# Kernel tuning notes

Measured on AMD Instinct MI355X. Metric: run time of the kernel, lower is better.

Reference implementation:

```python
import jax, jax.numpy as jnp
import numpy as np

N = 100000
E = 1600000
IN_C = 256
HID = 128
OUT_C = 128
HEADS = 4
C_HEAD = HID // HEADS
BN_EPS = 1e-5
NEG_SLOPE = 0.2


def setup_inputs() -> dict:
    key = jax.random.key(0)
    ks = jax.random.split(key, 12)
    s = lambda fan: 1.0 / np.sqrt(fan)
    return {
        "x": jax.random.normal(ks[0], (N, IN_C), dtype=jnp.float32),
        "W_gat": jax.random.normal(ks[1], (IN_C, HID), dtype=jnp.float32) * s(IN_C),
        "att_src": jax.random.normal(ks[2], (HEADS, C_HEAD), dtype=jnp.float32) * s(C_HEAD),
        "att_dst": jax.random.normal(ks[3], (HEADS, C_HEAD), dtype=jnp.float32) * s(C_HEAD),
        "bias_gat": jnp.zeros((HID,), dtype=jnp.float32),
        "bn1_gamma": jnp.ones((HID,), dtype=jnp.float32),
        "bn1_beta": jnp.zeros((HID,), dtype=jnp.float32),
        "eps_gin": jnp.zeros((), dtype=jnp.float32),
        "lin_W": jax.random.normal(ks[4], (HID, OUT_C), dtype=jnp.float32) * s(HID),
        "lin_b": jnp.zeros((OUT_C,), dtype=jnp.float32),
        "bn2_gamma": jnp.ones((OUT_C,), dtype=jnp.float32),
        "bn2_beta": jnp.zeros((OUT_C,), dtype=jnp.float32),
        "edge_index": jax.random.randint(ks[5], (2, E), 0, N, dtype=jnp.int64),
    }


def batch_norm(h, gamma, beta):
    mu = jnp.mean(h, axis=0)
    var = jnp.var(h, axis=0)
    return (h - mu) * jax.lax.rsqrt(var + BN_EPS) * gamma + beta


def reference(x, W_gat, att_src, att_dst, bias_gat, bn1_gamma, bn1_beta,
              eps_gin, lin_W, lin_b, bn2_gamma, bn2_beta, edge_index):
    src, dst = edge_index[0], edge_index[1]
    # ---- GATConv ----
    h = (x @ W_gat).reshape(N, HEADS, C_HEAD)              # [N,H,C]
    a_src = jnp.einsum('nhc,hc->nh', h, att_src)            # [N,H]
    a_dst = jnp.einsum('nhc,hc->nh', h, att_dst)            # [N,H]
    e = jax.nn.leaky_relu(a_src[src] + a_dst[dst], NEG_SLOPE)  # [E,H]
    # segment softmax over incoming edges of each dst node
    m = jax.ops.segment_max(e, dst, num_segments=N)         # [N,H]
    num = jnp.exp(e - m[dst])                                # [E,H]
    den = jax.ops.segment_sum(num, dst, num_segments=N)      # [N,H]
    alpha = num / den[dst]                                   # [E,H]
    msg = alpha[:, :, None] * h[src]                         # [E,H,C]
    out1 = jax.ops.segment_sum(msg, dst, num_segments=N)     # [N,H,C]
    out1 = out1.reshape(N, HID) + bias_gat
    # BN + ELU (dropout = identity in eval)
    out1 = jax.nn.elu(batch_norm(out1, bn1_gamma, bn1_beta))
    # ---- GINConv: nn((1+eps)*x + sum_neighbors) ----
    agg = jax.ops.segment_sum(out1[src], dst, num_segments=N)
    z = (1.0 + eps_gin) * out1 + agg
    out2 = z @ lin_W + lin_b
    out2 = jax.nn.elu(batch_norm(out2, bn2_gamma, bn2_beta))
    return out2
```

## Files before the change

### kernel.cpp

```cpp
#include <hip/hip_runtime.h>

#define N_NODES 100000
#define N_EDGES 1600000
#define IN_C 256
#define HID 128
#define NEG_SLOPE 0.2f
#define BN_EPS 1e-5f
#define NBUCK 391
#define NPART 391
#define BPAD 5120
#define ELEM_BLOCKS 2048

typedef unsigned int uint32;
typedef __attribute__((ext_vector_type(8))) short bf16x8;
typedef __attribute__((ext_vector_type(4))) float f32x4;

__device__ __forceinline__ float lrelu(float x) { return x > 0.f ? x : NEG_SLOPE * x; }

__device__ __forceinline__ unsigned short f2bf(float f) {
    uint32 u = __float_as_uint(f);
    u += 0x7fffu + ((u >> 16) & 1u);
    return (unsigned short)(u >> 16);
}
__device__ __forceinline__ float bf2f(unsigned short h) {
    return __uint_as_float(((uint32)h) << 16);
}
__device__ __forceinline__ float bflo(uint32 v) { return __uint_as_float(v << 16); }
__device__ __forceinline__ float bfhi(uint32 v) { return __uint_as_float(v & 0xffff0000u); }
__device__ __forceinline__ uint32 packbf(float a, float b) {
    return (uint32)f2bf(a) | ((uint32)f2bf(b) << 16);
}

__global__ void k_transpose_all(const float* __restrict__ W1, const float* __restrict__ W2,
                                unsigned short* __restrict__ Wt1,
                                unsigned short* __restrict__ Wt2,
                                int* __restrict__ gcursor, float* __restrict__ bnacc) {
    int t = threadIdx.x;
    if (blockIdx.x == 0) {
        for (int i = t; i < NBUCK + 1; i += 256) gcursor[i] = 0;
        bnacc[t] = 0.f;
        bnacc[256 + t] = 0.f;
    }
    int idx = blockIdx.x * 256 + t;
    if (idx < IN_C * 128) {
        int k = idx >> 7, n = idx & 127;
        Wt1[n * IN_C + k] = f2bf(W1[idx]);
    } else {
        idx -= IN_C * 128;
        if (idx < HID * 128) {
            int k = idx >> 7, n = idx & 127;
            Wt2[n * HID + k] = f2bf(W2[idx]);
        }
    }
}

template <bool AF32, bool OUTF32, bool ATT, bool STATS>
__global__ __launch_bounds__(256) void k_gemm(const void* __restrict__ Av,
                                              const unsigned short* __restrict__ Wt,
                                              void* __restrict__ Out, int K,
                                              const float* __restrict__ att_s,
                                              const float* __restrict__ att_d,
                                              float* __restrict__ a_src,
                                              float* __restrict__ a_dst,
                                              float* __restrict__ bnst) {
    __shared__ unsigned short As[128 * 72];
    __shared__ unsigned short Bs[128 * 72];
    const int t = threadIdx.x;
    const int n0 = blockIdx.x * 128;
    const int wv = t >> 6, lane = t & 63;
    const int wy = wv >> 1, wx = wv & 1;
    const int lm = lane & 15, lg = lane >> 4;
    const float* Af = (const float*)Av;
    const unsigned short* Ah = (const unsigned short*)Av;

    f32x4 acc[4][4];
#pragma unroll
    for (int i = 0; i < 4; ++i)
#pragma unroll
        for (int j = 0; j < 4; ++j) acc[i][j] = (f32x4){0.f, 0.f, 0.f, 0.f};

    float4 afp[8];
    uint4 ahp[4];
    uint4 bvp[4];

    if (AF32) {
#pragma unroll
        for (int p = 0; p < 8; ++p) {
            int idx = p * 256 + t, row = idx >> 4, c4 = idx & 15, gn = n0 + row;
            afp[p] = (gn < N_NODES) ? *(const float4*)&Af[(size_t)gn * K + c4 * 4]
                                    : make_float4(0.f, 0.f, 0.f, 0.f);
        }
    } else {
#pragma unroll
        for (int p = 0; p < 4; ++p) {
            int idx = p * 256 + t, row = idx >> 3, c = idx & 7, gn = n0 + row;
            ahp[p] = (gn < N_NODES) ? *(const uint4*)&Ah[(size_t)gn * K + c * 8]
                                    : make_uint4(0, 0, 0, 0);
        }
    }
#pragma unroll
    for (int p = 0; p < 4; ++p) {
        int idx = p * 256 + t, n = idx >> 3, c = idx & 7;
        bvp[p] = *(const uint4*)&Wt[(size_t)n * K + c * 8];
    }

    for (int kc = 0; kc < K; kc += 64) {
        if (AF32) {
#pragma unroll
            for (int p = 0; p < 8; ++p) {
                int idx = p * 256 + t, row = idx >> 4, c4 = idx & 15;
                ushort4 b;
                b.x = f2bf(afp[p].x); b.y = f2bf(afp[p].y);
                b.z = f2bf(afp[p].z); b.w = f2bf(afp[p].w);
                *(ushort4*)&As[row * 72 + c4 * 4] = b;
            }
        } else {
#pragma unroll
            for (int p = 0; p < 4; ++p) {
                int idx = p * 256 + t, row = idx >> 3, c = idx & 7;
                *(uint4*)&As[row * 72 + c * 8] = ahp[p];
            }
        }
#pragma unroll
        for (int p = 0; p < 4; ++p) {
            int idx = p * 256 + t, n = idx >> 3, c = idx & 7;
            *(uint4*)&Bs[n * 72 + c * 8] = bvp[p];
        }
        __syncthreads();
        int kn = kc + 64;
        if (kn < K) {
            if (AF32) {
#pragma unroll
                for (int p = 0; p < 8; ++p) {
                    int idx = p * 256 + t, row = idx >> 4, c4 = idx & 15, gn = n0 + row;
                    afp[p] = (gn < N_NODES) ? *(const float4*)&Af[(size_t)gn * K + kn + c4 * 4]
                                            : make_float4(0.f, 0.f, 0.f, 0.f);
                }
            } else {
#pragma unroll
                for (int p = 0; p < 4; ++p) {
                    int idx = p * 256 + t, row = idx >> 3, c = idx & 7, gn = n0 + row;
                    ahp[p] = (gn < N_NODES) ? *(const uint4*)&Ah[(size_t)gn * K + kn + c * 8]
                                            : make_uint4(0, 0, 0, 0);
                }
            }
#pragma unroll
            for (int p = 0; p < 4; ++p) {
                int idx = p * 256 + t, n = idx >> 3, c = idx & 7;
                bvp[p] = *(const uint4*)&Wt[(size_t)n * K + kn + c * 8];
            }
        }
#pragma unroll
        for (int ks = 0; ks < 2; ++ks) {
            bf16x8 af[4], bfr[4];
#pragma unroll
            for (int i = 0; i < 4; ++i)
                af[i] = *(const bf16x8*)&As[(wy * 64 + i * 16 + lm) * 72 + ks * 32 + lg * 8];
#pragma unroll
            for (int j = 0; j < 4; ++j)
                bfr[j] = *(const bf16x8*)&Bs[(wx * 64 + j * 16 + lm) * 72 + ks * 32 + lg * 8];
#pragma unroll
            for (int i = 0; i < 4; ++i)
#pragma unroll
                for (int j = 0; j < 4; ++j)
                    acc[i][j] = __builtin_amdgcn_mfma_f32_16x16x32_bf16(af[i], bfr[j],
                                                                        acc[i][j], 0, 0, 0);
        }
        __syncthreads();
    }

    float as_w[4], ad_w[4];
    if (ATT) {
#pragma unroll
        for (int j = 0; j < 4; ++j) {
            int col = wx * 64 + j * 16 + lm;
            as_w[j] = att_s[col];
            ad_w[j] = att_d[col];
        }
    }
    float ls[4] = {0.f, 0.f, 0.f, 0.f}, lq[4] = {0.f, 0.f, 0.f, 0.f};
#pragma unroll
    for (int i = 0; i < 4; ++i) {
#pragma unroll
        for (int r = 0; r < 4; ++r) {
            int row = n0 + wy * 64 + i * 16 + lg * 4 + r;
            float v0 = acc[i][0][r], v1 = acc[i][1][r];
            float v2 = acc[i][2][r], v3 = acc[i][3][r];
            if (row < N_NODES) {
                if (OUTF32) {
                    float* op = (float*)Out + (size_t)row * 128 + wx * 64 + lm;
                    op[0] = v0; op[16] = v1; op[32] = v2; op[48] = v3;
                } else {
                    unsigned short* op =
                        (unsigned short*)Out + (size_t)row * 128 + wx * 64 + lm;
                    op[0] = f2bf(v0); op[16] = f2bf(v1);
                    op[32] = f2bf(v2); op[48] = f2bf(v3);
                }
            }
            if (STATS) {
                ls[0] += v0; lq[0] += v0 * v0;
                ls[1] += v1; lq[1] += v1 * v1;
                ls[2] += v2; lq[2] += v2 * v2;
                ls[3] += v3; lq[3] += v3 * v3;
            }
            if (ATT) {
                float ps0 = v0 * as_w[0] + v1 * as_w[1];
                float ps1 = v2 * as_w[2] + v3 * as_w[3];
                float pd0 = v0 * ad_w[0] + v1 * ad_w[1];
                float pd1 = v2 * ad_w[2] + v3 * ad_w[3];
#pragma unroll
                for (int m = 1; m < 16; m <<= 1) {
                    ps0 += __shfl_xor(ps0, m); ps1 += __shfl_xor(ps1, m);
                    pd0 += __shfl_xor(pd0, m); pd1 += __shfl_xor(pd1, m);
                }
                if (lm == 0 && row < N_NODES) {
                    *(float2*)&a_src[row * 4 + wx * 2] = make_float2(ps0, ps1);
                    *(float2*)&a_dst[row * 4 + wx * 2] = make_float2(pd0, pd1);
                }
            }
        }
    }
    if (STATS) {
#pragma unroll
        for (int j = 0; j < 4; ++j) {
            float s = ls[j], q = lq[j];
            s += __shfl_xor(s, 16); s += __shfl_xor(s, 32);
            q += __shfl_xor(q, 16); q += __shfl_xor(q, 32);
            if (lg == 0) {
                int col = wx * 64 + j * 16 + lm;
                atomicAdd(&bnst[col], s);
                atomicAdd(&bnst[128 + col], q);
            }
        }
    }
}

__global__ __launch_bounds__(256) void k_partition(const int* __restrict__ ei,
                                                   int* __restrict__ gcursor,
                                                   int* __restrict__ staging) {
    __shared__ int hist[NBUCK];
    __shared__ int base[NBUCK];
    int t = threadIdx.x;
    int e0 = blockIdx.x * 4096;
    for (int i = t; i < NBUCK; i += 256) hist[i] = 0;
    __syncthreads();
    int pk[16], cb[16];
#pragma unroll
    for (int u = 0; u < 16; ++u) {
        int e = e0 + u * 256 + t;
        cb[u] = -1;
        if (e < N_EDGES) {
            int s = ei[e], d = ei[N_EDGES + e];
            int b = d >> 8;
            int r = atomicAdd(&hist[b], 1);
            pk[u] = ((d & 255) << 17) | s;
            cb[u] = (r << 9) | b;
        }
    }
    __syncthreads();
    for (int i = t; i < NBUCK; i += 256)
        if (hist[i]) base[i] = atomicAdd(&gcursor[i], hist[i]);
    __syncthreads();
#pragma unroll
    for (int u = 0; u < 16; ++u) {
        if (cb[u] >= 0) {
            int b = cb[u] & 511, r = cb[u] >> 9;
            staging[b * BPAD + base[b] + r] = pk[u];
        }
    }
}

__global__ void k_bucket_scan(const int* __restrict__ cnts, int* __restrict__ bucket_base,
                              int* __restrict__ row_ptr) {
    __shared__ int sh[512];
    int t = threadIdx.x;
    int v0 = (t < NBUCK) ? cnts[t] : 0;
    int val = v0;
    sh[t] = val;
    __syncthreads();
    for (int off = 1; off < 512; off <<= 1) {
        int o = (t >= off) ? sh[t - off] : 0;
        __syncthreads();
        val += o;
        sh[t] = val;
        __syncthreads();
    }
    if (t < NBUCK) bucket_base[t] = val - v0;
    if (t == 0) row_ptr[N_NODES] = N_EDGES;
}

__global__ __launch_bounds__(256) void k_bucket_sort(const int* __restrict__ staging,
                                                     const int* __restrict__ cnts,
                                                     const int* __restrict__ bucket_base,
                                                     int* __restrict__ row_ptr,
                                                     int* __restrict__ sorted_src) {
    __shared__ int hist[256];
    __shared__ int sh[256];
    __shared__ int spill[256][2];
    __shared__ int spill_cnt;
    int t = threadIdx.x, b = blockIdx.x;
    int cnt = cnts[b];
    int ob = bucket_base[b];
    const int* sb = staging + b * BPAD;
    hist[t] = 0;
    if (t == 0) spill_cnt = 0;
    __syncthreads();
    int ent[18], rnk[18];
#pragma unroll
    for (int u = 0; u < 18; ++u) {
        int i = u * 256 + t;
        ent[u] = -1;
        rnk[u] = 0;
        if (i < cnt) {
            int p = sb[i];
            ent[u] = p;
            rnk[u] = atomicAdd(&hist[p >> 17], 1);
        }
    }
    for (int i = 18 * 256 + t; i < cnt; i += 256) {
        int p = sb[i];
        int r = atomicAdd(&hist[p >> 17], 1);
        int si = atomicAdd(&spill_cnt, 1);
        spill[si][0] = p;
        spill[si][1] = r;
    }
    __syncthreads();
    int v0 = hist[t];
    int val = v0;
    sh[t] = val;
    __syncthreads();
    for (int off = 1; off < 256; off <<= 1) {
        int o = (t >= off) ? sh[t - off] : 0;
        __syncthreads();
        val += o;
        sh[t] = val;
        __syncthreads();
    }
    int excl = val - v0;
    int d = b * 256 + t;
    if (d < N_NODES) row_ptr[d] = ob + excl;
    __syncthreads();
    hist[t] = excl;
    __syncthreads();
#pragma unroll
    for (int u = 0; u < 18; ++u) {
        if (ent[u] >= 0) {
            int p = ent[u];
            sorted_src[ob + hist[p >> 17] + rnk[u]] = p & 0x1FFFF;
        }
    }
    for (int i = t; i < spill_cnt; i += 256) {
        int p = spill[i][0];
        sorted_src[ob + hist[p >> 17] + spill[i][1]] = p & 0x1FFFF;
    }
}

__global__ __launch_bounds__(256) void k_gat_agg(const uint32* __restrict__ h32,
                                                 const float* __restrict__ a_src,
                                                 const float* __restrict__ a_dst,
                                                 const int* __restrict__ row_ptr,
                                                 const int* __restrict__ sorted_src,
                                                 uint32* __restrict__ out1) {
    __shared__ alignas(16) float wbuf[4][4][72];
    int lane = threadIdx.x & 63, wv = threadIdx.x >> 6;
    int hd = lane >> 4;
    int node = blockIdx.x * 4 + wv;
    int start = row_ptr[node];
    int deg = row_ptr[node + 1] - start;
    if (deg == 0) {
        out1[((uint32)node << 6) + lane] = 0u;
        return;
    }
    float4 ad = *(const float4*)&a_dst[node * 4];
    float acc0 = 0.f, acc1 = 0.f, den = 0.f;
    for (int j0 = 0; j0 < deg; j0 += 64) {
        int m = min(64, deg - j0);
        int s = 0;
        float4 w = make_float4(0.f, 0.f, 0.f, 0.f);
        if (lane < m) {
            s = sorted_src[start + j0 + lane];
            float4 as = *(const float4*)&a_src[s * 4];
            w.x = __expf(lrelu(as.x + ad.x));
            w.y = __expf(lrelu(as.y + ad.y));
            w.z = __expf(lrelu(as.z + ad.z));
            w.w = __expf(lrelu(as.w + ad.w));
        }
        wbuf[wv][0][lane] = w.x;
        wbuf[wv][1][lane] = w.y;
        wbuf[wv][2][lane] = w.z;
        wbuf[wv][3][lane] = w.w;
        __builtin_amdgcn_wave_barrier();
        int e0 = 0;
        for (; e0 + 8 <= m; e0 += 8) {
            uint32 hr[8];
#pragma unroll
            for (int k = 0; k < 8; ++k) {
                int ss = __builtin_amdgcn_readlane(s, e0 + k);
                hr[k] = h32[((uint32)ss << 6) + lane];
            }
            float4 w0 = *(const float4*)&wbuf[wv][hd][e0];
            float4 w1 = *(const float4*)&wbuf[wv][hd][e0 + 4];
            float wk[8] = {w0.x, w0.y, w0.z, w0.w, w1.x, w1.y, w1.z, w1.w};
#pragma unroll
            for (int k = 0; k < 8; ++k) {
                den += wk[k];
                acc0 = fmaf(wk[k], bflo(hr[k]), acc0);
                acc1 = fmaf(wk[k], bfhi(hr[k]), acc1);
            }
        }
        for (; e0 < m; ++e0) {
            int ss = __builtin_amdgcn_readlane(s, e0);
            uint32 hv = h32[((uint32)ss << 6) + lane];
            float wk = wbuf[wv][hd][e0];
            den += wk;
            acc0 = fmaf(wk, bflo(hv), acc0);
            acc1 = fmaf(wk, bfhi(hv), acc1);
        }
        __builtin_amdgcn_wave_barrier();
    }
    float rden = 1.f / den;
    out1[((uint32)node << 6) + lane] = packbf(acc0 * rden, acc1 * rden);
}

__global__ __launch_bounds__(256) void k_gin_agg(const uint32* __restrict__ ob,
                                                 const int* __restrict__ row_ptr,
                                                 const int* __restrict__ sorted_src,
                                                 const float* __restrict__ eps_ptr,
                                                 uint32* __restrict__ zb) {
    int lane = threadIdx.x & 63, wv = threadIdx.x >> 6;
    int node = blockIdx.x * 4 + wv;
    int start = row_ptr[node];
    int deg = row_ptr[node + 1] - start;
    float acc0 = 0.f, acc1 = 0.f;
    for (int j0 = 0; j0 < deg; j0 += 64) {
        int m = min(64, deg - j0);
        int s = 0;
        if (lane < m) s = sorted_src[start + j0 + lane];
        int e0 = 0;
        for (; e0 + 8 <= m; e0 += 8) {
            uint32 hr[8];
#pragma unroll
            for (int k = 0; k < 8; ++k) {
                int ss = __builtin_amdgcn_readlane(s, e0 + k);
                hr[k] = ob[((uint32)ss << 6) + lane];
            }
#pragma unroll
            for (int k = 0; k < 8; ++k) {
                acc0 += bflo(hr[k]);
                acc1 += bfhi(hr[k]);
            }
        }
        for (; e0 < m; ++e0) {
            int ss = __builtin_amdgcn_readlane(s, e0);
            uint32 hv = ob[((uint32)ss << 6) + lane];
            acc0 += bflo(hv);
            acc1 += bfhi(hv);
        }
    }
    float ep = 1.f + eps_ptr[0];
    uint32 own = ob[((uint32)node << 6) + lane];
    zb[((uint32)node << 6) + lane] = packbf(fmaf(ep, bflo(own), acc0),
                                            fmaf(ep, bfhi(own), acc1));
}

__global__ __launch_bounds__(256) void k_bnstats_bf16(const uint32* __restrict__ buf,
                                                      float* __restrict__ acc) {
    __shared__ float sh[4][64][4];
    int lane = threadIdx.x & 63, grp = threadIdx.x >> 6;
    float s0 = 0.f, s1 = 0.f, q0 = 0.f, q1 = 0.f;
    for (int r = blockIdx.x * 4 + grp; r < N_NODES; r += gridDim.x * 4) {
        uint32 v = buf[(size_t)r * 64 + lane];
        float v0 = bflo(v), v1 = bfhi(v);
        s0 += v0; s1 += v1; q0 += v0 * v0; q1 += v1 * v1;
    }
    sh[grp][lane][0] = s0; sh[grp][lane][1] = s1;
    sh[grp][lane][2] = q0; sh[grp][lane][3] = q1;
    __syncthreads();
    if (grp == 0) {
#pragma unroll
        for (int g = 1; g < 4; ++g) {
            s0 += sh[g][lane][0]; s1 += sh[g][lane][1];
            q0 += sh[g][lane][2]; q1 += sh[g][lane][3];
        }
        int c0 = lane * 2;
        atomicAdd(&acc[c0], s0);
        atomicAdd(&acc[c0 + 1], s1);
        atomicAdd(&acc[128 + c0], q0);
        atomicAdd(&acc[128 + c0 + 1], q1);
    }
}

__global__ __launch_bounds__(256) void k_bn_elu_b16(uint32* __restrict__ buf,
                                                    const float* __restrict__ acc,
                                                    const float* __restrict__ gamma,
                                                    const float* __restrict__ beta) {
    int t = threadIdx.x;
    int c0 = (t & 63) * 2;
    float mu0 = acc[c0] * (1.f / N_NODES), mu1 = acc[c0 + 1] * (1.f / N_NODES);
    float va0 = acc[128 + c0] * (1.f / N_NODES) - mu0 * mu0;
    float va1 = acc[128 + c0 + 1] * (1.f / N_NODES) - mu1 * mu1;
    float s0 = rsqrtf(va0 + BN_EPS) * gamma[c0];
    float s1 = rsqrtf(va1 + BN_EPS) * gamma[c0 + 1];
    float h0 = beta[c0] - mu0 * s0;
    float h1 = beta[c0 + 1] - mu1 * s1;
    for (size_t i = (size_t)blockIdx.x * 256 + t; i < (size_t)N_NODES * 64;
         i += (size_t)ELEM_BLOCKS * 256) {
        uint32 v = buf[i];
        float r0 = fmaf(bflo(v), s0, h0);
        float r1 = fmaf(bfhi(v), s1, h1);
        r0 = r0 > 0.f ? r0 : __expf(r0) - 1.f;
        r1 = r1 > 0.f ? r1 : __expf(r1) - 1.f;
        buf[i] = packbf(r0, r1);
    }
}

__global__ __launch_bounds__(256) void k_bn_elu_out(const uint32* __restrict__ in,
                                                    const float* __restrict__ acc,
                                                    const float* __restrict__ gamma,
                                                    const float* __restrict__ beta,
                                                    float2* __restrict__ out) {
    int t = threadIdx.x;
    int c0 = (t & 63) * 2;
    float mu0 = acc[c0] * (1.f / N_NODES), mu1 = acc[c0 + 1] * (1.f / N_NODES);
    float va0 = acc[128 + c0] * (1.f / N_NODES) - mu0 * mu0;
    float va1 = acc[128 + c0 + 1] * (1.f / N_NODES) - mu1 * mu1;
    float s0 = rsqrtf(va0 + BN_EPS) * gamma[c0];
    float s1 = rsqrtf(va1 + BN_EPS) * gamma[c0 + 1];
    float h0 = beta[c0] - mu0 * s0;
    float h1 = beta[c0 + 1] - mu1 * s1;
    for (size_t i = (size_t)blockIdx.x * 256 + t; i < (size_t)N_NODES * 64;
         i += (size_t)ELEM_BLOCKS * 256) {
        uint32 v = in[i];
        float r0 = fmaf(bflo(v), s0, h0);
        float r1 = fmaf(bfhi(v), s1, h1);
        r0 = r0 > 0.f ? r0 : __expf(r0) - 1.f;
        r1 = r1 > 0.f ? r1 : __expf(r1) - 1.f;
        out[i] = make_float2(r0, r1);
    }
}

extern "C" void kernel_launch(void* const* d_in, const int* in_sizes, int n_in,
                              void* d_out, int out_size, void* d_ws, size_t ws_size,
                              hipStream_t stream) {
    (void)in_sizes; (void)n_in; (void)out_size; (void)ws_size;
    const float* x       = (const float*)d_in[0];
    const float* W_gat   = (const float*)d_in[1];
    const float* att_src = (const float*)d_in[2];
    const float* att_dst = (const float*)d_in[3];
    const float* bn1_g   = (const float*)d_in[5];
    const float* bn1_b   = (const float*)d_in[6];
    const float* eps_gin = (const float*)d_in[7];
    const float* lin_W   = (const float*)d_in[8];
    const float* bn2_g   = (const float*)d_in[10];
    const float* bn2_b   = (const float*)d_in[11];
    const int*   ei      = (const int*)d_in[12];
    float* out = (float*)d_out;

    char* w = (char*)d_ws;
    size_t o = 0;
    auto take = [&](size_t b) -> char* {
        char* p = w + o;
        o += (b + 255) & ~(size_t)255;
        return p;
    };
    unsigned short* hb   = (unsigned short*)take((size_t)N_NODES * 128 * 2);
    unsigned short* Wt1  = (unsigned short*)take((size_t)128 * IN_C * 2);
    unsigned short* Wt2  = (unsigned short*)take((size_t)128 * HID * 2);
    uint32* o1b          = (uint32*)take((size_t)N_NODES * 64 * 4);
    float* a_src         = (float*)take((size_t)N_NODES * 4 * 4);
    float* a_dst         = (float*)take((size_t)N_NODES * 4 * 4);
    int*   sorted        = (int*)take((size_t)N_EDGES * 4);
    int*   staging       = (int*)take((size_t)NBUCK * BPAD * 4);
    int*   row_ptr       = (int*)take((size_t)(N_NODES + 1) * 4);
    int*   bucket_base   = (int*)take((NBUCK + 1) * 4);
    int*   gcursor       = (int*)take((NBUCK + 1) * 4);
    float* bnacc         = (float*)take(512 * 4);
    uint32* zb  = (uint32*)hb;
    uint32* o2b = o1b;

    const int nGemmBlocks = (N_NODES + 127) / 128;

    k_transpose_all<<<((IN_C + HID) * 128 + 255) / 256, 256, 0, stream>>>(
        W_gat, lin_W, Wt1, Wt2, gcursor, bnacc);
    k_gemm<true, false, true, false><<<nGemmBlocks, 256, 0, stream>>>(
        x, Wt1, hb, IN_C, att_src, att_dst, a_src, a_dst, nullptr);
    k_partition<<<NPART, 256, 0, stream>>>(ei, gcursor, staging);
    k_bucket_scan<<<1, 512, 0, stream>>>(gcursor, bucket_base, row_ptr);
    k_bucket_sort<<<NBUCK, 256, 0, stream>>>(staging, gcursor, bucket_base, row_ptr,
                                             sorted);
    k_gat_agg<<<N_NODES / 4, 256, 0, stream>>>((const uint32*)hb, a_src, a_dst, row_ptr,
                                               sorted, o1b);
    k_bnstats_bf16<<<512, 256, 0, stream>>>(o1b, bnacc);
    k_bn_elu_b16<<<ELEM_BLOCKS, 256, 0, stream>>>(o1b, bnacc, bn1_g, bn1_b);
    k_gin_agg<<<N_NODES / 4, 256, 0, stream>>>(o1b, row_ptr, sorted, eps_gin, zb);
    k_gemm<false, false, false, true><<<nGemmBlocks, 256, 0, stream>>>(
        zb, Wt2, o2b, HID, nullptr, nullptr, nullptr, nullptr, bnacc + 256);
    k_bn_elu_out<<<ELEM_BLOCKS, 256, 0, stream>>>(o2b, bnacc + 256, bn2_g, bn2_b,
                                                  (float2*)out);
}
```

Baseline: 497.3 us.

## Fuse BN1+ELU into GIN aggregation, drop bucket scan kernel, coalesce partition writes

Removes the standalone BN1+ELU elementwise pass and instead applies the normalization and ELU on the fly to each gathered neighbor row and to the node's own row in the GIN aggregation. This saves one full read/write pass over the hidden features. The cost is recomputing exp for every edge gather, about 16 times more ELU work. The separate bucket-scan kernel is also removed: each sort block computes its own bucket offset by summing the preceding counts, and row_ptr's sentinel moves to the first kernel. The partition kernel now stages entries in shared memory, sorted by bucket, so its global scatter writes are more contiguous.

```diff
diff --git a/kernel.cpp b/kernel.cpp
--- a/kernel.cpp
+++ b/kernel.cpp
@@ -8,6 +8,7 @@
 #define BN_EPS 1e-5f
 #define NBUCK 391
 #define NPART 391
+#define PART_E 4096
 #define BPAD 5120
 #define ELEM_BLOCKS 2048
 
@@ -34,12 +35,14 @@
 __global__ void k_transpose_all(const float* __restrict__ W1, const float* __restrict__ W2,
                                 unsigned short* __restrict__ Wt1,
                                 unsigned short* __restrict__ Wt2,
-                                int* __restrict__ gcursor, float* __restrict__ bnacc) {
+                                int* __restrict__ gcursor, float* __restrict__ bnacc,
+                                int* __restrict__ row_ptr) {
     int t = threadIdx.x;
     if (blockIdx.x == 0) {
         for (int i = t; i < NBUCK + 1; i += 256) gcursor[i] = 0;
         bnacc[t] = 0.f;
         bnacc[256 + t] = 0.f;
+        if (t == 0) row_ptr[N_NODES] = N_EDGES;
     }
     int idx = blockIdx.x * 256 + t;
     if (idx < IN_C * 128) {
@@ -239,72 +242,85 @@
                                                    int* __restrict__ gcursor,
                                                    int* __restrict__ staging) {
     __shared__ int hist[NBUCK];
-    __shared__ int base[NBUCK];
+    __shared__ int loff[NBUCK];
+    __shared__ int gbase[NBUCK];
+    __shared__ int lstage[PART_E];
+    __shared__ int gaddr[PART_E];
+    __shared__ int scanbuf[512];
     int t = threadIdx.x;
-    int e0 = blockIdx.x * 4096;
+    int e0 = blockIdx.x * PART_E;
+    int cntAll = min(PART_E, N_EDGES - e0);
     for (int i = t; i < NBUCK; i += 256) hist[i] = 0;
     __syncthreads();
-    int pk[16], cb[16];
+    int pk[16];
+    short bb[16], rr[16];
 #pragma unroll
     for (int u = 0; u < 16; ++u) {
         int e = e0 + u * 256 + t;
-        cb[u] = -1;
+        bb[u] = -1;
+        rr[u] = 0;
         if (e < N_EDGES) {
             int s = ei[e], d = ei[N_EDGES + e];
             int b = d >> 8;
             int r = atomicAdd(&hist[b], 1);
             pk[u] = ((d & 255) << 17) | s;
-            cb[u] = (r << 9) | b;
-        }
-    }
-    __syncthreads();
-    for (int i = t; i < NBUCK; i += 256)
-        if (hist[i]) base[i] = atomicAdd(&gcursor[i], hist[i]);
+            bb[u] = (short)b;
+            rr[u] = (short)r;
+        }
+    }
+    __syncthreads();
+    scanbuf[t] = (t < NBUCK) ? hist[t] : 0;
+    scanbuf[t + 256] = (t + 256 < NBUCK) ? hist[t + 256] : 0;
+    __syncthreads();
+    for (int off = 1; off < 512; off <<= 1) {
+        int a0 = scanbuf[t];
+        int a1 = scanbuf[t + 256];
+        int b0 = (t >= off) ? scanbuf[t - off] : 0;
+        int b1 = (t + 256 >= off) ? scanbuf[t + 256 - off] : 0;
+        __syncthreads();
+        scanbuf[t] = a0 + b0;
+        scanbuf[t + 256] = a1 + b1;
+        __syncthreads();
+    }
+    for (int i = t; i < NBUCK; i += 256) {
+        loff[i] = scanbuf[i] - hist[i];
+        gbase[i] = hist[i] ? atomicAdd(&gcursor[i], hist[i]) : 0;
+    }
     __syncthreads();
 #pragma unroll
     for (int u = 0; u < 16; ++u) {
-        if (cb[u] >= 0) {
-            int b = cb[u] & 511, r = cb[u] >> 9;
-            staging[b * BPAD + base[b] + r] = pk[u];
-        }
-    }
-}
-
-__global__ void k_bucket_scan(const int* __restrict__ cnts, int* __restrict__ bucket_base,
-                              int* __restrict__ row_ptr) {
-    __shared__ int sh[512];
-    int t = threadIdx.x;
-    int v0 = (t < NBUCK) ? cnts[t] : 0;
-    int val = v0;
-    sh[t] = val;
-    __syncthreads();
-    for (int off = 1; off < 512; off <<= 1) {
-        int o = (t >= off) ? sh[t - off] : 0;
-        __syncthreads();
-        val += o;
-        sh[t] = val;
-        __syncthreads();
-    }
-    if (t < NBUCK) bucket_base[t] = val - v0;
-    if (t == 0) row_ptr[N_NODES] = N_EDGES;
+        if (bb[u] >= 0) {
+            int b = bb[u], r = rr[u];
+            int pos = loff[b] + r;
+            lstage[pos] = pk[u];
+            gaddr[pos] = b * BPAD + gbase[b] + r;
+        }
+    }
+    __syncthreads();
+    for (int i = t; i < cntAll; i += 256) staging[gaddr[i]] = lstage[i];
 }
 
 __global__ __launch_bounds__(256) void k_bucket_sort(const int* __restrict__ staging,
                                                      const int* __restrict__ cnts,
-                                                     const int* __restrict__ bucket_base,
                                                      int* __restrict__ row_ptr,
                                                      int* __restrict__ sorted_src) {
     __shared__ int hist[256];
     __shared__ int sh[256];
     __shared__ int spill[256][2];
     __shared__ int spill_cnt;
+    __shared__ int obs[4];
     int t = threadIdx.x, b = blockIdx.x;
+    int part = 0;
+    for (int i = t; i < b; i += 256) part += cnts[i];
+#pragma unroll
+    for (int m = 1; m < 64; m <<= 1) part += __shfl_xor(part, m);
+    if ((t & 63) == 0) obs[t >> 6] = part;
     int cnt = cnts[b];
-    int ob = bucket_base[b];
-    const int* sb = staging + b * BPAD;
     hist[t] = 0;
     if (t == 0) spill_cnt = 0;
     __syncthreads();
+    int ob = obs[0] + obs[1] + obs[2] + obs[3];
+    const int* sb = staging + b * BPAD;
     int ent[18], rnk[18];
 #pragma unroll
     for (int u = 0; u < 18; ++u) {
@@ -426,8 +442,19 @@
                                                  const int* __restrict__ row_ptr,
                                                  const int* __restrict__ sorted_src,
                                                  const float* __restrict__ eps_ptr,
+                                                 const float* __restrict__ acc_,
+                                                 const float* __restrict__ gamma,
+                                                 const float* __restrict__ beta,
                                                  uint32* __restrict__ zb) {
     int lane = threadIdx.x & 63, wv = threadIdx.x >> 6;
+    int c0 = lane * 2;
+    float mu0 = acc_[c0] * (1.f / N_NODES), mu1 = acc_[c0 + 1] * (1.f / N_NODES);
+    float va0 = acc_[128 + c0] * (1.f / N_NODES) - mu0 * mu0;
+    float va1 = acc_[128 + c0 + 1] * (1.f / N_NODES) - mu1 * mu1;
+    float s0 = rsqrtf(va0 + BN_EPS) * gamma[c0];
+    float s1 = rsqrtf(va1 + BN_EPS) * gamma[c0 + 1];
+    float h0 = beta[c0] - mu0 * s0;
+    float h1 = beta[c0 + 1] - mu1 * s1;
     int node = blockIdx.x * 4 + wv;
     int start = row_ptr[node];
     int deg = row_ptr[node + 1] - start;
@@ -446,21 +473,28 @@
             }
 #pragma unroll
             for (int k = 0; k < 8; ++k) {
-                acc0 += bflo(hr[k]);
-                acc1 += bfhi(hr[k]);
+                float f0 = fmaf(bflo(hr[k]), s0, h0);
+                float f1 = fmaf(bfhi(hr[k]), s1, h1);
+                acc0 += f0 > 0.f ? f0 : __expf(f0) - 1.f;
+                acc1 += f1 > 0.f ? f1 : __expf(f1) - 1.f;
             }
         }
         for (; e0 < m; ++e0) {
             int ss = __builtin_amdgcn_readlane(s, e0);
             uint32 hv = ob[((uint32)ss << 6) + lane];
-            acc0 += bflo(hv);
-            acc1 += bfhi(hv);
+            float f0 = fmaf(bflo(hv), s0, h0);
+            float f1 = fmaf(bfhi(hv), s1, h1);
+            acc0 += f0 > 0.f ? f0 : __expf(f0) - 1.f;
+            acc1 += f1 > 0.f ? f1 : __expf(f1) - 1.f;
         }
     }
     float ep = 1.f + eps_ptr[0];
     uint32 own = ob[((uint32)node << 6) + lane];
-    zb[((uint32)node << 6) + lane] = packbf(fmaf(ep, bflo(own), acc0),
-                                            fmaf(ep, bfhi(own), acc1));
+    float f0 = fmaf(bflo(own), s0, h0);
+    float f1 = fmaf(bfhi(own), s1, h1);
+    f0 = f0 > 0.f ? f0 : __expf(f0) - 1.f;
+    f1 = f1 > 0.f ? f1 : __expf(f1) - 1.f;
+    zb[((uint32)node << 6) + lane] = packbf(fmaf(ep, f0, acc0), fmaf(ep, f1, acc1));
 }
 
 __global__ __launch_bounds__(256) void k_bnstats_bf16(const uint32* __restrict__ buf,
@@ -487,30 +521,6 @@
         atomicAdd(&acc[c0 + 1], s1);
         atomicAdd(&acc[128 + c0], q0);
         atomicAdd(&acc[128 + c0 + 1], q1);
-    }
-}
-
-__global__ __launch_bounds__(256) void k_bn_elu_b16(uint32* __restrict__ buf,
-                                                    const float* __restrict__ acc,
-                                                    const float* __restrict__ gamma,
-                                                    const float* __restrict__ beta) {
-    int t = threadIdx.x;
-    int c0 = (t & 63) * 2;
-    float mu0 = acc[c0] * (1.f / N_NODES), mu1 = acc[c0 + 1] * (1.f / N_NODES);
-    float va0 = acc[128 + c0] * (1.f / N_NODES) - mu0 * mu0;
-    float va1 = acc[128 + c0 + 1] * (1.f / N_NODES) - mu1 * mu1;
-    float s0 = rsqrtf(va0 + BN_EPS) * gamma[c0];
-    float s1 = rsqrtf(va1 + BN_EPS) * gamma[c0 + 1];
-    float h0 = beta[c0] - mu0 * s0;
-    float h1 = beta[c0 + 1] - mu1 * s1;
-    for (size_t i = (size_t)blockIdx.x * 256 + t; i < (size_t)N_NODES * 64;
-         i += (size_t)ELEM_BLOCKS * 256) {
-        uint32 v = buf[i];
-        float r0 = fmaf(bflo(v), s0, h0);
-        float r1 = fmaf(bfhi(v), s1, h1);
-        r0 = r0 > 0.f ? r0 : __expf(r0) - 1.f;
-        r1 = r1 > 0.f ? r1 : __expf(r1) - 1.f;
-        buf[i] = packbf(r0, r1);
     }
 }
 
@@ -572,27 +582,23 @@
     int*   sorted        = (int*)take((size_t)N_EDGES * 4);
     int*   staging       = (int*)take((size_t)NBUCK * BPAD * 4);
     int*   row_ptr       = (int*)take((size_t)(N_NODES + 1) * 4);
-    int*   bucket_base   = (int*)take((NBUCK + 1) * 4);
     int*   gcursor       = (int*)take((NBUCK + 1) * 4);
     float* bnacc         = (float*)take(512 * 4);
     uint32* zb  = (uint32*)hb;
     uint32* o2b = o1b;
-
     const int nGemmBlocks = (N_NODES + 127) / 128;
 
     k_transpose_all<<<((IN_C + HID) * 128 + 255) / 256, 256, 0, stream>>>(
-        W_gat, lin_W, Wt1, Wt2, gcursor, bnacc);
+        W_gat, lin_W, Wt1, Wt2, gcursor, bnacc, row_ptr);
     k_gemm<true, false, true, false><<<nGemmBlocks, 256, 0, stream>>>(
         x, Wt1, hb, IN_C, att_src, att_dst, a_src, a_dst, nullptr);
     k_partition<<<NPART, 256, 0, stream>>>(ei, gcursor, staging);
-    k_bucket_scan<<<1, 512, 0, stream>>>(gcursor, bucket_base, row_ptr);
-    k_bucket_sort<<<NBUCK, 256, 0, stream>>>(staging, gcursor, bucket_base, row_ptr,
-                                             sorted);
+    k_bucket_sort<<<NBUCK, 256, 0, stream>>>(staging, gcursor, row_ptr, sorted);
     k_gat_agg<<<N_NODES / 4, 256, 0, stream>>>((const uint32*)hb, a_src, a_dst, row_ptr,
                                                sorted, o1b);
     k_bnstats_bf16<<<512, 256, 0, stream>>>(o1b, bnacc);
-    k_bn_elu_b16<<<ELEM_BLOCKS, 256, 0, stream>>>(o1b, bnacc, bn1_g, bn1_b);
-    k_gin_agg<<<N_NODES / 4, 256, 0, stream>>>(o1b, row_ptr, sorted, eps_gin, zb);
+    k_gin_agg<<<N_NODES / 4, 256, 0, stream>>>(o1b, row_ptr, sorted, eps_gin, bnacc,
+                                               bn1_g, bn1_b, zb);
     k_gemm<false, false, false, true><<<nGemmBlocks, 256, 0, stream>>>(
         zb, Wt2, o2b, HID, nullptr, nullptr, nullptr, nullptr, bnacc + 256);
     k_bn_elu_out<<<ELEM_BLOCKS, 256, 0, stream>>>(o2b, bnacc + 256, bn2_g, bn2_b,
```

Result: no change. 501.0 us (+0.7%).
